# Optimization experiments

Measured on AMD Instinct MI355X. Metric: run time of the kernel, lower is better.

## Reference

```python
import jax, jax.numpy as jnp
import numpy as np
from jax import lax

K = 3  # kernel_size
DN = ('NCHW', 'OIHW', 'NCHW')


def _conv(x, w, b, pad):
    out = lax.conv_general_dilated(x, w, window_strides=(1, 1),
                                   padding=((pad, pad), (pad, pad)),
                                   dimension_numbers=DN)
    return out + b[None, :, None, None]


def setup_inputs() -> dict:
    key = jax.random.key(0)
    ks = jax.random.split(key, 6)
    N, C, H, W = 8, 64, 128, 128
    x = jax.random.normal(ks[0], (N, C, H, W), dtype=jnp.float32)
    y = jax.random.normal(ks[1], (N, C, H, W), dtype=jnp.float32)
    w1 = jax.random.normal(ks[2], (C, C, 3, 3), dtype=jnp.float32) * 0.05
    b1 = jax.random.normal(ks[3], (C,), dtype=jnp.float32) * 0.05
    w2 = jax.random.normal(ks[4], (C * K * K, C, 1, 1), dtype=jnp.float32) * 0.05
    b2 = jax.random.normal(ks[5], (C * K * K,), dtype=jnp.float32) * 0.05
    return {"x": x, "y": y, "w1": w1, "b1": b1, "w2": w2, "b2": b2}


def reference(x, y, w1, b1, w2, b2):
    N, C, H, W = x.shape
    # kernel generation: 3x3 conv (C->C) then 1x1 conv (C -> C*9)
    h = _conv(y, w1, b1, pad=1)
    kernel = _conv(h, w2, b2, pad=0).reshape(N, C, K * K, H, W)
    # unfold x (3x3, pad 1): patch ordering (kh, kw) row-major per channel,
    # matching nn.Unfold's (C, kh, kw) channel layout after the reshape.
    xp = jnp.pad(x, ((0, 0), (0, 0), (1, 1), (1, 1)))
    patches = jnp.stack([xp[:, :, i:i + H, j:j + W]
                         for i in range(K) for j in range(K)], axis=2)
    # per-pixel dynamic conv: elementwise multiply + reduce over the 9 taps
    return (patches * kernel).sum(axis=2)
```

## Files before the change

kernel.cpp:

```cpp
#include <hip/hip_runtime.h>

#define C   64
#define H   128
#define W   128
#define HW  (H * W)
#define NB  8

using bf16x8 = __attribute__((ext_vector_type(8))) short;
using f32x4  = __attribute__((ext_vector_type(4))) float;

__device__ __forceinline__ unsigned short f2bf(float f) {
    unsigned u = __float_as_uint(f);
    return (unsigned short)((u + 0x7fffu + ((u >> 16) & 1u)) >> 16);
}

__global__ __launch_bounds__(256) void prep_weights(
    const float* __restrict__ w1, const float* __restrict__ w2,
    const float* __restrict__ b2,
    unsigned short* __restrict__ w1f, unsigned short* __restrict__ w2f,
    float* __restrict__ b2f)
{
    int i = blockIdx.x * 256 + threadIdx.x;
    if (i < 36864) {
        {
            int j = i & 7, lane = (i >> 3) & 63, m = (i >> 9) & 3, s = i >> 11;
            int l15 = lane & 15, lhi = lane >> 4;
            int co = m * 16 + l15;
            int kk = s * 32 + lhi * 8 + j;
            int tap = kk >> 6, k = kk & 63;
            w1f[i] = f2bf(w1[co * 576 + k * 9 + tap]);
        }
        {
            int j = i & 7, lane = (i >> 3) & 63, ks = (i >> 9) & 1, t9 = i >> 10;
            int tap = t9 % 9, cc = t9 / 9;
            int cp = cc * 16 + (lane & 15);
            int k = ks * 32 + (lane >> 4) * 8 + j;
            w2f[i] = f2bf(w2[(cp * 9 + tap) * 64 + k]);
        }
    }
    if (i < 9216) {
        int r = i & 3, lane = (i >> 2) & 63, t9 = i >> 8;
        int tap = t9 % 9, cc = t9 / 9;
        int cpp = cc * 16 + ((lane >> 4) << 2) + r;
        b2f[i] = b2[cpp * 9 + tap];
    }
}

__global__ __launch_bounds__(256) void transpose_y(
    const float* __restrict__ y, unsigned short* __restrict__ yT)
{
    __shared__ unsigned short tl[64 * 64];
    const int t = threadIdx.x, b = blockIdx.x;
    const int n = b & 7, tile = b >> 3;
    const int px0 = tile * 64;
    const int wv = t >> 6, l = t & 63;

    const float* src = y + (size_t)n * C * HW + px0 + l;
    #pragma unroll
    for (int i = 0; i < 8; ++i) {
        int ch = wv * 16 + i * 2;
        float v0 = src[(size_t)ch * HW];
        float v1 = src[(size_t)(ch + 1) * HW];
        unsigned pk = (unsigned)f2bf(v0) | ((unsigned)f2bf(v1) << 16);
        *(unsigned*)&tl[l * 64 + (ch ^ ((l & 7) << 3))] = pk;
    }
    __syncthreads();

    const int px = t >> 2, c0 = (t & 3) * 16;
    const int xr = (px & 7) << 3;
    uint4 w0 = *(const uint4*)&tl[px * 64 + (c0 ^ xr)];
    uint4 w1 = *(const uint4*)&tl[px * 64 + ((c0 + 8) ^ xr)];
    unsigned short* dst = yT + ((size_t)n * HW + px0 + px) * 64 + c0;
    *(uint4*)&dst[0] = w0;
    *(uint4*)&dst[8] = w1;
}

__global__ __launch_bounds__(256, 1) void fused_dc(
    const float* __restrict__ x,
    const unsigned short* __restrict__ yT,
    const unsigned short* __restrict__ w1f,
    const float* __restrict__ b1,
    const unsigned short* __restrict__ w2f,
    const float* __restrict__ b2f,
    float* __restrict__ out)
{
    __shared__ unsigned short h_lds[4 * 128 * 64];

    const int t = threadIdx.x, b = blockIdx.x;
    const int n = b & 7;
    const int wid = t >> 6, lane = t & 63;
    const int l15 = lane & 15, lhi = lane >> 4;
    const int p = ((b >> 3) << 2) + wid;

    const unsigned short* yTn = yT + (size_t)n * HW * 64;
    unsigned short* h_my = &h_lds[wid * 128 * 64];

    {
        f32x4 acc[4][8];
        #pragma unroll
        for (int m = 0; m < 4; ++m)
            #pragma unroll
            for (int pt = 0; pt < 8; ++pt)
                acc[m][pt] = f32x4{0.f, 0.f, 0.f, 0.f};

        #pragma unroll
        for (int s = 0; s < 18; ++s) {
            const int tap = s >> 1, trow = tap / 3, dq = tap % 3 - 1;
            const int k0 = (s & 1) * 32 + lhi * 8;
            const int grow = p + trow - 1;
            const bool rok = (unsigned)grow < (unsigned)H;
            const int cg = rok ? grow : 0;

            bf16x8 Y[8];
            #pragma unroll
            for (int pt = 0; pt < 8; ++pt) {
                int col = pt * 16 + l15 + dq;
                bool ok = rok && ((unsigned)col < (unsigned)W);
                int cl = col < 0 ? 0 : (col > 127 ? 127 : col);
                bf16x8 v = *(const bf16x8*)&yTn[((size_t)cg * W + cl) * 64 + k0];
                Y[pt] = ok ? v : (bf16x8)0;
            }
            bf16x8 Wf[4];
            #pragma unroll
            for (int m = 0; m < 4; ++m)
                Wf[m] = *(const bf16x8*)&w1f[(size_t)((s * 4 + m) * 64 + lane) * 8];

            #pragma unroll
            for (int m = 0; m < 4; ++m)
                #pragma unroll
                for (int pt = 0; pt < 8; ++pt)
                    acc[m][pt] = __builtin_amdgcn_mfma_f32_16x16x32_bf16(
                        Wf[m], Y[pt], acc[m][pt], 0, 0, 0);
        }

        #pragma unroll
        for (int m = 0; m < 4; ++m) {
            float4 bq = *(const float4*)&b1[m * 16 + lhi * 4];
            #pragma unroll
            for (int pt = 0; pt < 8; ++pt) {
                int px = pt * 16 + l15;
                int cb = m * 16 + lhi * 4;
                unsigned lo = (unsigned)f2bf(acc[m][pt][0] + bq.x)
                            | ((unsigned)f2bf(acc[m][pt][1] + bq.y) << 16);
                unsigned hi = (unsigned)f2bf(acc[m][pt][2] + bq.z)
                            | ((unsigned)f2bf(acc[m][pt][3] + bq.w) << 16);
                uint2 pk; pk.x = lo; pk.y = hi;
                *(uint2*)&h_my[px * 64 + (cb ^ ((px & 7) << 3))] = pk;
            }
        }
    }

    bf16x8 hA[8][2];
    #pragma unroll
    for (int pt = 0; pt < 8; ++pt)
        #pragma unroll
        for (int ks = 0; ks < 2; ++ks) {
            int px = pt * 16 + l15;
            int ko = ks * 32 + lhi * 8;
            hA[pt][ks] = *(const bf16x8*)&h_my[px * 64 + (ko ^ ((px & 7) << 3))];
        }

    const float* xn_ = x + (size_t)n * C * HW;
    float* out_ = out + (size_t)n * C * HW;

    #pragma unroll
    for (int cc = 0; cc < 4; ++cc) {
        bf16x8 wA0[2], wA1[2];
        f32x4  bq[2];
        float  xv[2][8][4];

        auto loadTap = [&](int tap, int bi) {
            const int t9 = cc * 9 + tap;
            wA0[bi] = *(const bf16x8*)&w2f[(size_t)((t9 * 2 + 0) * 64 + lane) * 8];
            wA1[bi] = *(const bf16x8*)&w2f[(size_t)((t9 * 2 + 1) * 64 + lane) * 8];
            bq[bi]  = *(const f32x4*)&b2f[(size_t)(t9 * 64 + lane) * 4];
            const int ri = tap / 3, cj = tap % 3;
            const int grow = p + ri - 1;
            const bool rok = (unsigned)grow < (unsigned)H;
            const int cr = rok ? grow : 0;
            #pragma unroll
            for (int pt = 0; pt < 8; ++pt) {
                int col = pt * 16 + l15 + cj - 1;
                bool ok = rok && ((unsigned)col < (unsigned)W);
                int cl = col < 0 ? 0 : (col > 127 ? 127 : col);
                const float* xb = xn_ + (size_t)(cc * 16 + lhi * 4) * HW
                                + (size_t)cr * W + cl;
                #pragma unroll
                for (int r = 0; r < 4; ++r) {
                    float v = xb[(size_t)r * HW];
                    xv[bi][pt][r] = ok ? v : 0.f;
                }
            }
        };

        f32x4 oacc[8];
        #pragma unroll
        for (int pt = 0; pt < 8; ++pt) oacc[pt] = f32x4{0.f, 0.f, 0.f, 0.f};

        loadTap(0, 0);
        #pragma unroll
        for (int tap = 0; tap < 9; ++tap) {
            if (tap < 8) loadTap(tap + 1, (tap + 1) & 1);
            const int bi = tap & 1;
            #pragma unroll
            for (int pt = 0; pt < 8; ++pt) {
                f32x4 kf = __builtin_amdgcn_mfma_f32_16x16x32_bf16(
                    wA0[bi], hA[pt][0], bq[bi], 0, 0, 0);
                kf = __builtin_amdgcn_mfma_f32_16x16x32_bf16(
                    wA1[bi], hA[pt][1], kf, 0, 0, 0);
                #pragma unroll
                for (int r = 0; r < 4; ++r)
                    oacc[pt][r] = fmaf(kf[r], xv[bi][pt][r], oacc[pt][r]);
            }
        }

        #pragma unroll
        for (int pt = 0; pt < 8; ++pt)
            #pragma unroll
            for (int r = 0; r < 4; ++r)
                out_[(size_t)(cc * 16 + lhi * 4 + r) * HW
                     + (size_t)p * W + pt * 16 + l15] = oacc[pt][r];
    }
}

extern "C" void kernel_launch(void* const* d_in, const int* in_sizes, int n_in,
                              void* d_out, int out_size, void* d_ws, size_t ws_size,
                              hipStream_t stream)
{
    const float* x  = (const float*)d_in[0];
    const float* y  = (const float*)d_in[1];
    const float* w1 = (const float*)d_in[2];
    const float* b1 = (const float*)d_in[3];
    const float* w2 = (const float*)d_in[4];
    const float* b2 = (const float*)d_in[5];
    float* out = (float*)d_out;

    char* ws = (char*)d_ws;
    unsigned short* yT  = (unsigned short*)ws;
    unsigned short* w1f = (unsigned short*)(ws + 16777216);
    unsigned short* w2f = (unsigned short*)(ws + 16777216 + 73728);
    float*          b2f = (float*)(ws + 16777216 + 147456);

    prep_weights<<<144, 256, 0, stream>>>(w1, w2, b2, w1f, w2f, b2f);
    transpose_y<<<NB * HW / 64, 256, 0, stream>>>(y, yT);
    fused_dc<<<NB * H / 4, 256, 0, stream>>>(x, yT, w1f, b1, w2f, b2f, out);
}
```

Baseline: 66.51 us.

## Split each image row across two waves by output-channel half

Each row is now handled by two waves instead of one. Each wave computes half of the conv1 output channels into a shared LDS row buffer, then after a block barrier it handles half of the output channel groups in the dynamic-conv stage. The block count doubles, per-wave accumulators and LDS shrink, and the launch bound allows two blocks per CU, which should raise occupancy and parallelism. In exchange it adds a __syncthreads, and each row's y tile loads for conv1 are now done by two waves, doubling those global reads.

```diff
diff --git a/kernel.cpp b/kernel.cpp
--- a/kernel.cpp
+++ b/kernel.cpp
@@ -75,7 +75,7 @@
     *(uint4*)&dst[8] = w1;
 }
 
-__global__ __launch_bounds__(256, 1) void fused_dc(
+__global__ __launch_bounds__(256, 2) void fused_dc(
     const float* __restrict__ x,
     const unsigned short* __restrict__ yT,
     const unsigned short* __restrict__ w1f,
@@ -84,24 +84,26 @@
     const float* __restrict__ b2f,
     float* __restrict__ out)
 {
-    __shared__ unsigned short h_lds[4 * 128 * 64];
+    __shared__ unsigned short h_lds[2 * 128 * 64];
 
     const int t = threadIdx.x, b = blockIdx.x;
     const int n = b & 7;
     const int wid = t >> 6, lane = t & 63;
     const int l15 = lane & 15, lhi = lane >> 4;
-    const int p = ((b >> 3) << 2) + wid;
+    const int rsel = wid >> 1;
+    const int half = wid & 1;
+    const int p = (b >> 3) * 2 + rsel;
 
     const unsigned short* yTn = yT + (size_t)n * HW * 64;
-    unsigned short* h_my = &h_lds[wid * 128 * 64];
+    unsigned short* h_row = &h_lds[rsel * 128 * 64];
 
     {
-        f32x4 acc[4][8];
-        #pragma unroll
-        for (int m = 0; m < 4; ++m)
+        f32x4 acc[2][8];
+        #pragma unroll
+        for (int mi = 0; mi < 2; ++mi)
             #pragma unroll
             for (int pt = 0; pt < 8; ++pt)
-                acc[m][pt] = f32x4{0.f, 0.f, 0.f, 0.f};
+                acc[mi][pt] = f32x4{0.f, 0.f, 0.f, 0.f};
 
         #pragma unroll
         for (int s = 0; s < 18; ++s) {
@@ -120,35 +122,39 @@
                 bf16x8 v = *(const bf16x8*)&yTn[((size_t)cg * W + cl) * 64 + k0];
                 Y[pt] = ok ? v : (bf16x8)0;
             }
-            bf16x8 Wf[4];
-            #pragma unroll
-            for (int m = 0; m < 4; ++m)
-                Wf[m] = *(const bf16x8*)&w1f[(size_t)((s * 4 + m) * 64 + lane) * 8];
-
-            #pragma unroll
-            for (int m = 0; m < 4; ++m)
+            bf16x8 Wf[2];
+            #pragma unroll
+            for (int mi = 0; mi < 2; ++mi) {
+                int m = half * 2 + mi;
+                Wf[mi] = *(const bf16x8*)&w1f[(size_t)((s * 4 + m) * 64 + lane) * 8];
+            }
+
+            #pragma unroll
+            for (int mi = 0; mi < 2; ++mi)
                 #pragma unroll
                 for (int pt = 0; pt < 8; ++pt)
-                    acc[m][pt] = __builtin_amdgcn_mfma_f32_16x16x32_bf16(
-                        Wf[m], Y[pt], acc[m][pt], 0, 0, 0);
-        }
-
-        #pragma unroll
-        for (int m = 0; m < 4; ++m) {
+                    acc[mi][pt] = __builtin_amdgcn_mfma_f32_16x16x32_bf16(
+                        Wf[mi], Y[pt], acc[mi][pt], 0, 0, 0);
+        }
+
+        #pragma unroll
+        for (int mi = 0; mi < 2; ++mi) {
+            const int m = half * 2 + mi;
             float4 bq = *(const float4*)&b1[m * 16 + lhi * 4];
             #pragma unroll
             for (int pt = 0; pt < 8; ++pt) {
                 int px = pt * 16 + l15;
                 int cb = m * 16 + lhi * 4;
-                unsigned lo = (unsigned)f2bf(acc[m][pt][0] + bq.x)
-                            | ((unsigned)f2bf(acc[m][pt][1] + bq.y) << 16);
-                unsigned hi = (unsigned)f2bf(acc[m][pt][2] + bq.z)
-                            | ((unsigned)f2bf(acc[m][pt][3] + bq.w) << 16);
+                unsigned lo = (unsigned)f2bf(acc[mi][pt][0] + bq.x)
+                            | ((unsigned)f2bf(acc[mi][pt][1] + bq.y) << 16);
+                unsigned hi = (unsigned)f2bf(acc[mi][pt][2] + bq.z)
+                            | ((unsigned)f2bf(acc[mi][pt][3] + bq.w) << 16);
                 uint2 pk; pk.x = lo; pk.y = hi;
-                *(uint2*)&h_my[px * 64 + (cb ^ ((px & 7) << 3))] = pk;
-            }
-        }
-    }
+                *(uint2*)&h_row[px * 64 + (cb ^ ((px & 7) << 3))] = pk;
+            }
+        }
+    }
+    __syncthreads();
 
     bf16x8 hA[8][2];
     #pragma unroll
@@ -157,14 +163,15 @@
         for (int ks = 0; ks < 2; ++ks) {
             int px = pt * 16 + l15;
             int ko = ks * 32 + lhi * 8;
-            hA[pt][ks] = *(const bf16x8*)&h_my[px * 64 + (ko ^ ((px & 7) << 3))];
+            hA[pt][ks] = *(const bf16x8*)&h_row[px * 64 + (ko ^ ((px & 7) << 3))];
         }
 
     const float* xn_ = x + (size_t)n * C * HW;
     float* out_ = out + (size_t)n * C * HW;
 
     #pragma unroll
-    for (int cc = 0; cc < 4; ++cc) {
+    for (int j = 0; j < 2; ++j) {
+        const int cc = half * 2 + j;
         bf16x8 wA0[2], wA1[2];
         f32x4  bq[2];
         float  xv[2][8][4];
@@ -243,5 +250,5 @@
 
     prep_weights<<<144, 256, 0, stream>>>(w1, w2, b2, w1f, w2f, b2f);
     transpose_y<<<NB * HW / 64, 256, 0, stream>>>(y, yT);
-    fused_dc<<<NB * H / 4, 256, 0, stream>>>(x, yT, w1f, b1, w2f, b2f, out);
-}
+    fused_dc<<<NB * H / 2, 256, 0, stream>>>(x, yT, w1f, b1, w2f, b2f, out);
+}
```

After: 103.5 us. +55.6%, slower.
